# Kernel tuning notes

Hardware: AMD Instinct MI355X
Metric: run time of the kernel (lower is better)

The kernel has to match this reference:

```python
import jax, jax.numpy as jnp
import numpy as np

B, T, D = 2, 4096, 512
H = 8
HD = D // H  # 64


def setup_inputs() -> dict:
    key = jax.random.key(0)
    k1, k2, k3 = jax.random.split(key, 3)
    x = jax.random.normal(k1, (B, T, D), dtype=jnp.float32)
    w_qkv = jax.random.normal(k2, (3 * D, D), dtype=jnp.float32) * (1.0 / np.sqrt(D))
    w_out = jax.random.normal(k3, (D, D), dtype=jnp.float32) * (1.0 / np.sqrt(D))
    return {"x": x, "w_qkv": w_qkv, "w_out": w_out}


def reference(x, w_qkv, w_out):
    b, t, d = x.shape
    qkv = x @ w_qkv.T                      # [B,T,3D]
    q, k, v = jnp.split(qkv, 3, axis=-1)
    # b t (h d) -> b h t d
    def split_heads(a):
        return a.reshape(b, t, H, HD).transpose(0, 2, 1, 3)
    q, k, v = split_heads(q), split_heads(k), split_heads(v)
    scale = 1.0 / np.sqrt(HD).astype(np.float32)
    scores = jnp.einsum('bhqd,bhkd->bhqk', q, k) * scale  # [B,H,T,T]
    causal = jnp.tril(jnp.ones((t, t), dtype=bool))        # keep lower triangle
    scores = jnp.where(causal[None, None], scores, -jnp.inf)
    attn = jax.nn.softmax(scores, axis=-1)
    out = jnp.einsum('bhqk,bhkd->bhqd', attn, v)           # [B,H,T,HD]
    out = out.transpose(0, 2, 1, 3).reshape(b, t, d)       # b h t d -> b t (h d)
    return out @ w_out.T
```

## Files before the change

kernel.cpp:

```cpp
#include <hip/hip_runtime.h>
#include <hip/hip_bf16.h>

#define BB 2
#define TT 4096
#define DD 512
#define HH 8
#define HD 64
#define M_TOT (BB*TT)
#define N_QKV (3*DD)

typedef __attribute__((ext_vector_type(8))) __bf16 bf16x8;
typedef __attribute__((ext_vector_type(4))) float f32x4;

#define MFMA16(a,b,c) __builtin_amdgcn_mfma_f32_16x16x32_bf16((a),(b),(c),0,0,0)

#define SCALE_L2E 0.18033688011112443f
#define SHIFT_L2E 11.541560327111707f

static __device__ __forceinline__ unsigned short f2bf(float f) {
    union { float f; unsigned u; } v; v.f = f;
    return (unsigned short)((v.u + 0x8000u) >> 16);
}

static __device__ __forceinline__ bf16x8 load8(const unsigned short* p) {
    bf16x8 v;
    __builtin_memcpy(&v, p, 16);
    return v;
}

static __device__ __forceinline__ bf16x8 ones_frag() {
    unsigned short u[8];
    #pragma unroll
    for (int i = 0; i < 8; i++) u[i] = 0x3F80;
    bf16x8 v; __builtin_memcpy(&v, u, 16);
    return v;
}

#define GLDS(gp, lp) __builtin_amdgcn_global_load_lds( \
    (const __attribute__((address_space(1))) unsigned int*)(gp), \
    (__attribute__((address_space(3))) unsigned int*)(lp), 16, 0, 0)

#define NX4 (M_TOT*DD/4)
#define NW4 (N_QKV*DD/4)
#define NO4 (DD*DD/4)
__global__ __launch_bounds__(256) void cast_all(
        const float* __restrict__ x, const float* __restrict__ wqkv,
        const float* __restrict__ wout,
        unsigned short* __restrict__ xb, unsigned short* __restrict__ wqkvb,
        unsigned short* __restrict__ woutb) {
    int i = blockIdx.x * 256 + threadIdx.x;
    const float* s; unsigned short* d; int j;
    if (i < NX4)            { s = x;    d = xb;    j = i; }
    else if (i < NX4 + NW4) { s = wqkv; d = wqkvb; j = i - NX4; }
    else                    { s = wout; d = woutb; j = i - NX4 - NW4; }
    float4 f = ((const float4*)s)[j];
    ushort4 o;
    o.x = f2bf(f.x); o.y = f2bf(f.y); o.z = f2bf(f.z); o.w = f2bf(f.w);
    ((ushort4*)d)[j] = o;
}

__global__ __launch_bounds__(256) void qkv_gemm(
        const unsigned short* __restrict__ xb,
        const unsigned short* __restrict__ wb,
        unsigned short* __restrict__ qb,
        unsigned short* __restrict__ kb,
        unsigned short* __restrict__ vtb) {
    __shared__ unsigned short As[128 * 32];
    __shared__ unsigned short Bs[128 * 32];
    int tid = threadIdx.x;
    int w = tid >> 6, lane = tid & 63;
    int lrow = lane & 15, quad = lane >> 4;
    int bn = blockIdx.x % (N_QKV / 128);
    int bm = blockIdx.x / (N_QKV / 128);
    int m0 = bm * 128, n0 = bn * 128;
    int wm = w >> 1, wn = w & 1;

    f32x4 c[4][4];
    #pragma unroll
    for (int i = 0; i < 4; i++)
        #pragma unroll
        for (int j = 0; j < 4; j++) c[i][j] = (f32x4){0.f, 0.f, 0.f, 0.f};

    for (int k0 = 0; k0 < DD; k0 += 32) {
        #pragma unroll
        for (int j = 0; j < 2; j++) {
            int ch = j * 256 + tid;
            int row = ch >> 2, kc = ch & 3;
            GLDS(xb + (size_t)(m0 + row) * DD + k0 + kc * 8,
                 (char*)As + (size_t)(j * 256 + w * 64) * 16);
        }
        #pragma unroll
        for (int j = 0; j < 2; j++) {
            int ch = j * 256 + tid;
            int row = ch >> 2, kc = ch & 3;
            GLDS(wb + (size_t)(n0 + row) * DD + k0 + kc * 8,
                 (char*)Bs + (size_t)(j * 256 + w * 64) * 16);
        }
        __syncthreads();
        bf16x8 a[4], b[4];
        #pragma unroll
        for (int mf = 0; mf < 4; mf++) a[mf] = load8(&As[(wm * 64 + mf * 16 + lrow) * 32 + quad * 8]);
        #pragma unroll
        for (int nf = 0; nf < 4; nf++) b[nf] = load8(&Bs[(wn * 64 + nf * 16 + lrow) * 32 + quad * 8]);
        #pragma unroll
        for (int mf = 0; mf < 4; mf++)
            #pragma unroll
            for (int nf = 0; nf < 4; nf++)
                c[mf][nf] = MFMA16(a[mf], b[nf], c[mf][nf]);
        __syncthreads();
    }

    int m0w = m0 + wm * 64, n0w = n0 + wn * 64;
    int which = n0w >> 9;
    int h = (n0w & 511) >> 6;
    #pragma unroll
    for (int mf = 0; mf < 4; mf++) {
        #pragma unroll
        for (int r = 0; r < 4; r++) {
            int m = m0w + mf * 16 + quad * 4 + r;
            int t = m & (TT - 1), bi = m >> 12;
            size_t hb = (size_t)(bi * HH + h) * TT + t;
            #pragma unroll
            for (int nf = 0; nf < 4; nf++) {
                int d = nf * 16 + lrow;
                unsigned short val = f2bf(c[mf][nf][r]);
                if (which == 0)      qb[hb * HD + d] = val;
                else if (which == 1) kb[hb * HD + d] = val;
                else                 vtb[((size_t)(bi * HH + h) * HD + d) * TT + t] = val;
            }
        }
    }
}

__global__ __launch_bounds__(256) void attn_kernel(
        const unsigned short* __restrict__ qb,
        const unsigned short* __restrict__ kb,
        const unsigned short* __restrict__ vtb,
        unsigned short* __restrict__ attnb) {
    __shared__ union {
        unsigned short p[4][64][68];
        float c[2][64][66];
    } sm;

    int w = threadIdx.x >> 6;
    int lane = threadIdx.x & 63;
    int lrow = lane & 15, quad = lane >> 4;
    int bh = blockIdx.x & 15;
    int pr = blockIdx.x >> 4;
    int bi = bh >> 3, h = bh & 7;

    const unsigned short* qh = qb + (size_t)bh * TT * HD;
    const unsigned short* kh = kb + (size_t)bh * TT * HD;
    const unsigned short* vth = vtb + (size_t)bh * HD * TT;
    bf16x8 ones = ones_frag();

    for (int half = 0; half < 2; half++) {
        int qt = half ? (63 - pr) : pr;
        int q0 = qt * 64;

        bf16x8 qf[4][2];
        #pragma unroll
        for (int mf = 0; mf < 4; mf++) {
            const unsigned short* qp = qh + (q0 + mf * 16 + lrow) * HD + quad * 8;
            qf[mf][0] = load8(qp);
            qf[mf][1] = load8(qp + 32);
        }

        f32x4 o[4][4];
        f32x4 l[4];
        #pragma unroll
        for (int i = 0; i < 4; i++) {
            l[i] = (f32x4){0.f, 0.f, 0.f, 0.f};
            #pragma unroll
            for (int j = 0; j < 4; j++) o[i][j] = (f32x4){0.f, 0.f, 0.f, 0.f};
        }

        for (int kt = w; kt <= qt; kt += 4) {
            int kbase = kt * 64;
            bool diag = (kt == qt);
            #pragma unroll
            for (int nf = 0; nf < 4; nf++) {
                const unsigned short* kp = kh + (kbase + nf * 16 + lrow) * HD + quad * 8;
                bf16x8 kf0 = load8(kp);
                bf16x8 kf1 = load8(kp + 32);
                #pragma unroll
                for (int mf = 0; mf < 4; mf++) {
                    if (diag && nf > mf) {
                        #pragma unroll
                        for (int r = 0; r < 4; r++)
                            sm.p[w][mf * 16 + quad * 4 + r][nf * 16 + lrow] = 0;
                    } else {
                        f32x4 s = {0.f, 0.f, 0.f, 0.f};
                        s = MFMA16(qf[mf][0], kf0, s);
                        s = MFMA16(qf[mf][1], kf1, s);
                        #pragma unroll
                        for (int r = 0; r < 4; r++) {
                            float p = __builtin_amdgcn_exp2f(s[r] * SCALE_L2E - SHIFT_L2E);
                            if (diag && nf == mf && lrow > quad * 4 + r) p = 0.f;
                            sm.p[w][mf * 16 + quad * 4 + r][nf * 16 + lrow] = f2bf(p);
                        }
                    }
                }
            }
            bf16x8 vf[4][2];
            #pragma unroll
            for (int nfd = 0; nfd < 4; nfd++) {
                const unsigned short* vp = vth + (nfd * 16 + lrow) * TT + kbase + quad * 8;
                vf[nfd][0] = load8(vp);
                vf[nfd][1] = load8(vp + 32);
            }
            #pragma unroll
            for (int mf = 0; mf < 4; mf++) {
                bf16x8 pa0, pa1;
                __builtin_memcpy(&pa0, &sm.p[w][mf * 16 + lrow][quad * 8], 16);
                __builtin_memcpy(&pa1, &sm.p[w][mf * 16 + lrow][32 + quad * 8], 16);
                l[mf] = MFMA16(pa0, ones, l[mf]);
                l[mf] = MFMA16(pa1, ones, l[mf]);
                #pragma unroll
                for (int nfd = 0; nfd < 4; nfd++) {
                    o[mf][nfd] = MFMA16(pa0, vf[nfd][0], o[mf][nfd]);
                    o[mf][nfd] = MFMA16(pa1, vf[nfd][1], o[mf][nfd]);
                }
            }
        }

        __syncthreads();
        if (w >= 2) {
            int cb = w - 2;
            #pragma unroll
            for (int mf = 0; mf < 4; mf++)
                #pragma unroll
                for (int r = 0; r < 4; r++) {
                    int row = mf * 16 + quad * 4 + r;
                    #pragma unroll
                    for (int nfd = 0; nfd < 4; nfd++)
                        sm.c[cb][row][nfd * 16 + lrow] = o[mf][nfd][r];
                    if (lrow == 0) sm.c[cb][row][64] = l[mf][r];
                }
        }
        __syncthreads();
        if (w < 2) {
            #pragma unroll
            for (int mf = 0; mf < 4; mf++)
                #pragma unroll
                for (int r = 0; r < 4; r++) {
                    int row = mf * 16 + quad * 4 + r;
                    #pragma unroll
                    for (int nfd = 0; nfd < 4; nfd++)
                        sm.c[w][row][nfd * 16 + lrow] += o[mf][nfd][r];
                    if (lrow == 0) sm.c[w][row][64] += l[mf][r];
                }
        }
        __syncthreads();
        #pragma unroll
        for (int r = 0; r < 4; r++) {
            int row = w * 16 + quad * 4 + r;
            float lsum = sm.c[0][row][64] + sm.c[1][row][64];
            float inv = 1.0f / lsum;
            int t = q0 + row;
            size_t base = ((size_t)(bi * TT + t)) * DD + h * HD;
            #pragma unroll
            for (int nfd = 0; nfd < 4; nfd++) {
                int col = nfd * 16 + lrow;
                float v = (sm.c[0][row][col] + sm.c[1][row][col]) * inv;
                attnb[base + col] = f2bf(v);
            }
        }
        __syncthreads();
    }
}

__global__ __launch_bounds__(256) void proj_gemm(
        const unsigned short* __restrict__ ab,
        const unsigned short* __restrict__ wb,
        float* __restrict__ out) {
    __shared__ unsigned short As[128 * 32];
    __shared__ unsigned short Bs[128 * 32];
    int tid = threadIdx.x;
    int w = tid >> 6, lane = tid & 63;
    int lrow = lane & 15, quad = lane >> 4;
    int bn = blockIdx.x % (DD / 128);
    int bm = blockIdx.x / (DD / 128);
    int m0 = bm * 128, n0 = bn * 128;
    int wm = w >> 1, wn = w & 1;

    f32x4 c[4][4];
    #pragma unroll
    for (int i = 0; i < 4; i++)
        #pragma unroll
        for (int j = 0; j < 4; j++) c[i][j] = (f32x4){0.f, 0.f, 0.f, 0.f};

    for (int k0 = 0; k0 < DD; k0 += 32) {
        #pragma unroll
        for (int j = 0; j < 2; j++) {
            int ch = j * 256 + tid;
            int row = ch >> 2, kc = ch & 3;
            GLDS(ab + (size_t)(m0 + row) * DD + k0 + kc * 8,
                 (char*)As + (size_t)(j * 256 + w * 64) * 16);
        }
        #pragma unroll
        for (int j = 0; j < 2; j++) {
            int ch = j * 256 + tid;
            int row = ch >> 2, kc = ch & 3;
            GLDS(wb + (size_t)(n0 + row) * DD + k0 + kc * 8,
                 (char*)Bs + (size_t)(j * 256 + w * 64) * 16);
        }
        __syncthreads();
        bf16x8 a[4], b[4];
        #pragma unroll
        for (int mf = 0; mf < 4; mf++) a[mf] = load8(&As[(wm * 64 + mf * 16 + lrow) * 32 + quad * 8]);
        #pragma unroll
        for (int nf = 0; nf < 4; nf++) b[nf] = load8(&Bs[(wn * 64 + nf * 16 + lrow) * 32 + quad * 8]);
        #pragma unroll
        for (int mf = 0; mf < 4; mf++)
            #pragma unroll
            for (int nf = 0; nf < 4; nf++)
                c[mf][nf] = MFMA16(a[mf], b[nf], c[mf][nf]);
        __syncthreads();
    }

    #pragma unroll
    for (int mf = 0; mf < 4; mf++) {
        #pragma unroll
        for (int r = 0; r < 4; r++) {
            int m = m0 + wm * 64 + mf * 16 + quad * 4 + r;
            #pragma unroll
            for (int nf = 0; nf < 4; nf++) {
                int n = n0 + wn * 64 + nf * 16 + lrow;
                out[(size_t)m * DD + n] = c[mf][nf][r];
            }
        }
    }
}

extern "C" void kernel_launch(void* const* d_in, const int* in_sizes, int n_in,
                              void* d_out, int out_size, void* d_ws, size_t ws_size,
                              hipStream_t stream) {
    const float* x    = (const float*)d_in[0];
    const float* wqkv = (const float*)d_in[1];
    const float* wout = (const float*)d_in[2];
    float* out = (float*)d_out;

    char* ws = (char*)d_ws;
    unsigned short* xb    = (unsigned short*)ws; ws += (size_t)M_TOT * DD * 2;
    unsigned short* wqkvb = (unsigned short*)ws; ws += (size_t)N_QKV * DD * 2;
    unsigned short* woutb = (unsigned short*)ws; ws += (size_t)DD * DD * 2;
    unsigned short* qb    = (unsigned short*)ws; ws += (size_t)BB * HH * TT * HD * 2;
    unsigned short* kb    = (unsigned short*)ws; ws += (size_t)BB * HH * TT * HD * 2;
    unsigned short* vtb   = (unsigned short*)ws; ws += (size_t)BB * HH * HD * TT * 2;
    unsigned short* attnb = (unsigned short*)ws; ws += (size_t)M_TOT * DD * 2;

    cast_all<<<(NX4 + NW4 + NO4) / 256, 256, 0, stream>>>(x, wqkv, wout, xb, wqkvb, woutb);

    qkv_gemm<<<(M_TOT / 128) * (N_QKV / 128), 256, 0, stream>>>(xb, wqkvb, qb, kb, vtb);

    attn_kernel<<<512, 256, 0, stream>>>(qb, kb, vtb, attnb);

    proj_gemm<<<(M_TOT / 128) * (DD / 128), 256, 0, stream>>>(attnb, woutb, out);
}
```

Before: 190.6 us.

## Split attention KV range across two blocks and stage V-transpose stores through LDS

The attention grid doubles to 1024 blocks. Each block handles every eighth key tile, and the two segments write unnormalized partial outputs and row sums to an fp32 workspace. A new attn_norm kernel then combines them and writes bf16. The QKV GEMM transposes V through shared memory so the transposed stores are 16-byte coalesced instead of scattered 2-byte writes. V loads are hoisted ahead of the QK^T compute, and P uses truncating bf16 conversion. The split adds fp32 workspace traffic and an extra launch in exchange for more parallelism across compute units.

```diff
diff --git a/kernel.cpp b/kernel.cpp
--- a/kernel.cpp
+++ b/kernel.cpp
@@ -20,6 +20,10 @@
 static __device__ __forceinline__ unsigned short f2bf(float f) {
     union { float f; unsigned u; } v; v.f = f;
     return (unsigned short)((v.u + 0x8000u) >> 16);
+}
+static __device__ __forceinline__ unsigned short f2bf_t(float f) {
+    union { float f; unsigned u; } v; v.f = f;
+    return (unsigned short)(v.u >> 16);
 }
 
 static __device__ __forceinline__ bf16x8 load8(const unsigned short* p) {
@@ -65,8 +69,10 @@
         unsigned short* __restrict__ qb,
         unsigned short* __restrict__ kb,
         unsigned short* __restrict__ vtb) {
-    __shared__ unsigned short As[128 * 32];
-    __shared__ unsigned short Bs[128 * 32];
+    __shared__ union {
+        struct { unsigned short As[128 * 32]; unsigned short Bs[128 * 32]; } g;
+        unsigned short vt[4][64][72];
+    } sm;
     int tid = threadIdx.x;
     int w = tid >> 6, lane = tid & 63;
     int lrow = lane & 15, quad = lane >> 4;
@@ -87,21 +93,21 @@
             int ch = j * 256 + tid;
             int row = ch >> 2, kc = ch & 3;
             GLDS(xb + (size_t)(m0 + row) * DD + k0 + kc * 8,
-                 (char*)As + (size_t)(j * 256 + w * 64) * 16);
+                 (char*)sm.g.As + (size_t)(j * 256 + w * 64) * 16);
         }
         #pragma unroll
         for (int j = 0; j < 2; j++) {
             int ch = j * 256 + tid;
             int row = ch >> 2, kc = ch & 3;
             GLDS(wb + (size_t)(n0 + row) * DD + k0 + kc * 8,
-                 (char*)Bs + (size_t)(j * 256 + w * 64) * 16);
+                 (char*)sm.g.Bs + (size_t)(j * 256 + w * 64) * 16);
         }
         __syncthreads();
         bf16x8 a[4], b[4];
         #pragma unroll
-        for (int mf = 0; mf < 4; mf++) a[mf] = load8(&As[(wm * 64 + mf * 16 + lrow) * 32 + quad * 8]);
-        #pragma unroll
-        for (int nf = 0; nf < 4; nf++) b[nf] = load8(&Bs[(wn * 64 + nf * 16 + lrow) * 32 + quad * 8]);
+        for (int mf = 0; mf < 4; mf++) a[mf] = load8(&sm.g.As[(wm * 64 + mf * 16 + lrow) * 32 + quad * 8]);
+        #pragma unroll
+        for (int nf = 0; nf < 4; nf++) b[nf] = load8(&sm.g.Bs[(wn * 64 + nf * 16 + lrow) * 32 + quad * 8]);
         #pragma unroll
         for (int mf = 0; mf < 4; mf++)
             #pragma unroll
@@ -113,21 +119,39 @@
     int m0w = m0 + wm * 64, n0w = n0 + wn * 64;
     int which = n0w >> 9;
     int h = (n0w & 511) >> 6;
-    #pragma unroll
-    for (int mf = 0; mf < 4; mf++) {
-        #pragma unroll
-        for (int r = 0; r < 4; r++) {
-            int m = m0w + mf * 16 + quad * 4 + r;
-            int t = m & (TT - 1), bi = m >> 12;
-            size_t hb = (size_t)(bi * HH + h) * TT + t;
-            #pragma unroll
-            for (int nf = 0; nf < 4; nf++) {
-                int d = nf * 16 + lrow;
-                unsigned short val = f2bf(c[mf][nf][r]);
-                if (which == 0)      qb[hb * HD + d] = val;
-                else if (which == 1) kb[hb * HD + d] = val;
-                else                 vtb[((size_t)(bi * HH + h) * HD + d) * TT + t] = val;
-            }
+    if (which < 2) {
+        unsigned short* dst = (which == 0) ? qb : kb;
+        #pragma unroll
+        for (int mf = 0; mf < 4; mf++) {
+            #pragma unroll
+            for (int r = 0; r < 4; r++) {
+                int m = m0w + mf * 16 + quad * 4 + r;
+                int t = m & (TT - 1), bi = m >> 12;
+                size_t hb = (size_t)(bi * HH + h) * TT + t;
+                #pragma unroll
+                for (int nf = 0; nf < 4; nf++) {
+                    int d = nf * 16 + lrow;
+                    dst[hb * HD + d] = f2bf(c[mf][nf][r]);
+                }
+            }
+        }
+    } else {
+        #pragma unroll
+        for (int mf = 0; mf < 4; mf++)
+            #pragma unroll
+            for (int r = 0; r < 4; r++)
+                #pragma unroll
+                for (int nf = 0; nf < 4; nf++)
+                    sm.vt[w][nf * 16 + lrow][mf * 16 + quad * 4 + r] = f2bf(c[mf][nf][r]);
+        int bi = m0w >> 12, t0 = m0w & (TT - 1);
+        size_t hb = (size_t)(bi * HH + h) * HD;
+        #pragma unroll
+        for (int i = 0; i < 8; i++) {
+            int d = i * 8 + (lane >> 3);
+            int tc = (lane & 7) * 8;
+            bf16x8 v;
+            __builtin_memcpy(&v, &sm.vt[w][d][tc], 16);
+            __builtin_memcpy(vtb + (hb + d) * TT + t0 + tc, &v, 16);
         }
     }
 }
@@ -136,7 +160,7 @@
         const unsigned short* __restrict__ qb,
         const unsigned short* __restrict__ kb,
         const unsigned short* __restrict__ vtb,
-        unsigned short* __restrict__ attnb) {
+        float* __restrict__ ows, float* __restrict__ lws) {
     __shared__ union {
         unsigned short p[4][64][68];
         float c[2][64][66];
@@ -146,14 +170,16 @@
     int lane = threadIdx.x & 63;
     int lrow = lane & 15, quad = lane >> 4;
     int bh = blockIdx.x & 15;
-    int pr = blockIdx.x >> 4;
-    int bi = bh >> 3, h = bh & 7;
+    int pr = (blockIdx.x >> 4) & 31;
+    int seg = blockIdx.x >> 9;
 
     const unsigned short* qh = qb + (size_t)bh * TT * HD;
     const unsigned short* kh = kb + (size_t)bh * TT * HD;
     const unsigned short* vth = vtb + (size_t)bh * HD * TT;
     bf16x8 ones = ones_frag();
 
+    int kres = (seg * 4 + w + pr) & 7;
+
     for (int half = 0; half < 2; half++) {
         int qt = half ? (63 - pr) : pr;
         int q0 = qt * 64;
@@ -175,9 +201,16 @@
             for (int j = 0; j < 4; j++) o[i][j] = (f32x4){0.f, 0.f, 0.f, 0.f};
         }
 
-        for (int kt = w; kt <= qt; kt += 4) {
+        for (int kt = kres; kt <= qt; kt += 8) {
             int kbase = kt * 64;
             bool diag = (kt == qt);
+            bf16x8 vf[4][2];
+            #pragma unroll
+            for (int nfd = 0; nfd < 4; nfd++) {
+                const unsigned short* vp = vth + (nfd * 16 + lrow) * TT + kbase + quad * 8;
+                vf[nfd][0] = load8(vp);
+                vf[nfd][1] = load8(vp + 32);
+            }
             #pragma unroll
             for (int nf = 0; nf < 4; nf++) {
                 const unsigned short* kp = kh + (kbase + nf * 16 + lrow) * HD + quad * 8;
@@ -190,24 +223,17 @@
                         for (int r = 0; r < 4; r++)
                             sm.p[w][mf * 16 + quad * 4 + r][nf * 16 + lrow] = 0;
                     } else {
-                        f32x4 s = {0.f, 0.f, 0.f, 0.f};
-                        s = MFMA16(qf[mf][0], kf0, s);
-                        s = MFMA16(qf[mf][1], kf1, s);
+                        f32x4 sv = {0.f, 0.f, 0.f, 0.f};
+                        sv = MFMA16(qf[mf][0], kf0, sv);
+                        sv = MFMA16(qf[mf][1], kf1, sv);
                         #pragma unroll
                         for (int r = 0; r < 4; r++) {
-                            float p = __builtin_amdgcn_exp2f(s[r] * SCALE_L2E - SHIFT_L2E);
+                            float p = __builtin_amdgcn_exp2f(sv[r] * SCALE_L2E - SHIFT_L2E);
                             if (diag && nf == mf && lrow > quad * 4 + r) p = 0.f;
-                            sm.p[w][mf * 16 + quad * 4 + r][nf * 16 + lrow] = f2bf(p);
+                            sm.p[w][mf * 16 + quad * 4 + r][nf * 16 + lrow] = f2bf_t(p);
                         }
                     }
                 }
-            }
-            bf16x8 vf[4][2];
-            #pragma unroll
-            for (int nfd = 0; nfd < 4; nfd++) {
-                const unsigned short* vp = vth + (nfd * 16 + lrow) * TT + kbase + quad * 8;
-                vf[nfd][0] = load8(vp);
-                vf[nfd][1] = load8(vp + 32);
             }
             #pragma unroll
             for (int mf = 0; mf < 4; mf++) {
@@ -252,22 +278,46 @@
                 }
         }
         __syncthreads();
+        size_t tbase = ((size_t)(bh * 64 + qt) * 2 + seg) * 64;
         #pragma unroll
         for (int r = 0; r < 4; r++) {
             int row = w * 16 + quad * 4 + r;
-            float lsum = sm.c[0][row][64] + sm.c[1][row][64];
-            float inv = 1.0f / lsum;
-            int t = q0 + row;
-            size_t base = ((size_t)(bi * TT + t)) * DD + h * HD;
+            if (lrow == 0)
+                lws[tbase + row] = sm.c[0][row][64] + sm.c[1][row][64];
             #pragma unroll
             for (int nfd = 0; nfd < 4; nfd++) {
                 int col = nfd * 16 + lrow;
-                float v = (sm.c[0][row][col] + sm.c[1][row][col]) * inv;
-                attnb[base + col] = f2bf(v);
-            }
-        }
-        __syncthreads();
-    }
+                ows[(tbase + row) * 64 + col] = sm.c[0][row][col] + sm.c[1][row][col];
+            }
+        }
+        __syncthreads();
+    }
+}
+
+__global__ __launch_bounds__(256) void attn_norm(
+        const float* __restrict__ ows, const float* __restrict__ lws,
+        unsigned short* __restrict__ attnb) {
+    int g = blockIdx.x;
+    int bh = g >> 6, qt = g & 63;
+    int bi = bh >> 3, h = bh & 7;
+    int row = threadIdx.x >> 2, dg = threadIdx.x & 3;
+    size_t r0 = ((size_t)g * 2 + 0) * 64 + row;
+    size_t r1 = r0 + 64;
+    float inv = 1.0f / (lws[r0] + lws[r1]);
+    const float4* p0 = (const float4*)(ows + r0 * 64 + dg * 16);
+    const float4* p1 = (const float4*)(ows + r1 * 64 + dg * 16);
+    int t = qt * 64 + row;
+    unsigned short* dst = attnb + ((size_t)(bi * TT + t)) * DD + h * HD + dg * 16;
+    ushort4 outv[4];
+    #pragma unroll
+    for (int j = 0; j < 4; j++) {
+        float4 a = p0[j], b = p1[j];
+        outv[j].x = f2bf_t((a.x + b.x) * inv);
+        outv[j].y = f2bf_t((a.y + b.y) * inv);
+        outv[j].z = f2bf_t((a.z + b.z) * inv);
+        outv[j].w = f2bf_t((a.w + b.w) * inv);
+    }
+    __builtin_memcpy(dst, outv, 32);
 }
 
 __global__ __launch_bounds__(256) void proj_gemm(
@@ -349,12 +399,16 @@
     unsigned short* kb    = (unsigned short*)ws; ws += (size_t)BB * HH * TT * HD * 2;
     unsigned short* vtb   = (unsigned short*)ws; ws += (size_t)BB * HH * HD * TT * 2;
     unsigned short* attnb = (unsigned short*)ws; ws += (size_t)M_TOT * DD * 2;
+    float* ows = (float*)ws; ws += (size_t)1024 * 2 * 64 * 64 * 4;
+    float* lws = (float*)ws; ws += (size_t)1024 * 2 * 64 * 4;
 
     cast_all<<<(NX4 + NW4 + NO4) / 256, 256, 0, stream>>>(x, wqkv, wout, xb, wqkvb, woutb);
 
     qkv_gemm<<<(M_TOT / 128) * (N_QKV / 128), 256, 0, stream>>>(xb, wqkvb, qb, kb, vtb);
 
-    attn_kernel<<<512, 256, 0, stream>>>(qb, kb, vtb, attnb);
+    attn_kernel<<<1024, 256, 0, stream>>>(qb, kb, vtb, ows, lws);
+
+    attn_norm<<<1024, 256, 0, stream>>>(ows, lws, attnb);
 
     proj_gemm<<<(M_TOT / 128) * (DD / 128), 256, 0, stream>>>(attnb, woutb, out);
 }
```

Result: slower. 202.0 us (+6.0%).
